# Performance work log

Hardware: AMD Instinct MI355X
Metric: run time of the kernel (lower is better)

## Reference

```python
import jax, jax.numpy as jnp
import numpy as np

N = 50000      # nodes
E = 1600000    # edges (avg degree 32)
F_IN = 512     # in_channels
H = 128        # hidden_channels


def setup_inputs() -> dict:
    key = jax.random.key(0)
    k0, k1, k2, k3 = jax.random.split(key, 4)
    x = jax.random.normal(k0, (N, F_IN), dtype=jnp.float32)
    edge_index = jax.random.randint(k1, (2, E), 0, N, dtype=jnp.int32)
    edge_weight = jnp.ones((E,), dtype=jnp.float32)
    # GCNConv weight (glorot) + bias, Linear weight (xavier) + bias.
    # Stored as [in, out] for direct matmul (same math as torch's x @ W.T).
    W_conv = jax.random.normal(k2, (F_IN, H), dtype=jnp.float32) * np.sqrt(2.0 / (F_IN + H)).astype(np.float32)
    b_conv = jnp.zeros((H,), dtype=jnp.float32)
    W_lin = jax.random.normal(k3, (H, F_IN), dtype=jnp.float32) * np.sqrt(2.0 / (H + F_IN)).astype(np.float32)
    b_lin = jnp.zeros((F_IN,), dtype=jnp.float32)
    return {
        "x": x, "edge_index": edge_index, "edge_weight": edge_weight,
        "W_conv": W_conv, "b_conv": b_conv, "W_lin": W_lin, "b_lin": b_lin,
    }


def reference(x, edge_index, edge_weight, W_conv, b_conv, W_lin, b_lin):
    n = x.shape[0]
    src, dst = edge_index[0], edge_index[1]
    # GCN normalization with self-loops (add_self_loops + sym norm)
    loop = jnp.arange(n, dtype=edge_index.dtype)
    src_f = jnp.concatenate([src, loop])            # [E+N]
    dst_f = jnp.concatenate([dst, loop])
    w = jnp.concatenate([edge_weight, jnp.ones((n,), x.dtype)])
    deg = jax.ops.segment_sum(w, dst_f, num_segments=n)  # [N]
    dinv = jnp.where(deg > 0, jax.lax.rsqrt(deg), 0.0)
    norm = dinv[src_f] * w * dinv[dst_f]            # [E+N]
    # GCNConv: transform then normalized neighbor aggregation
    h = x @ W_conv                                  # [N, H]
    agg = jax.ops.segment_sum(h[src_f] * norm[:, None], dst_f, num_segments=n) + b_conv  # [N, H]
    # dropout p=0.0 (eval) is identity; final linear projection back to F_IN
    return agg @ W_lin + b_lin                      # [N, F_IN]
```

## Files before the change

### kernel.cpp

```cpp
#include <hip/hip_runtime.h>

#define NN 50000
#define EE 1600000
#define FIN 512
#define HH 128

#define CAP 80
#define OVF_CAP 64512

#define GROUP 128
#define NB ((NN + GROUP - 1) / GROUP)
#define NBLK 256
#define EPB (EE / NBLK)

typedef short s16x8 __attribute__((ext_vector_type(8)));
typedef float f32x4 __attribute__((ext_vector_type(4)));

static __device__ inline unsigned short f2bf(float f) {
    unsigned u = __float_as_uint(f);
    unsigned r = (u + 0x7fffu + ((u >> 16) & 1u)) >> 16;
    return (unsigned short)r;
}

static __device__ inline float blo(unsigned u) { return __uint_as_float(u << 16); }
static __device__ inline float bhi(unsigned u) { return __uint_as_float(u & 0xffff0000u); }


__global__ __launch_bounds__(256) void hist_kernel(const int* __restrict__ dst,
                                                   int* __restrict__ hist) {
    __shared__ int h[NB];
    const int tid = threadIdx.x;
    for (int i = tid; i < NB; i += 256) h[i] = 0;
    __syncthreads();
    const int base = blockIdx.x * EPB;
    for (int i = tid; i < EPB; i += 256)
        atomicAdd(&h[dst[base + i] >> 7], 1);
    __syncthreads();
    for (int i = tid; i < NB; i += 256) hist[blockIdx.x * NB + i] = h[i];
}

__global__ __launch_bounds__(64) void scan_bins(const int* __restrict__ hist,
                                                int* __restrict__ off,
                                                int* __restrict__ binTotal) {
    const int bin = blockIdx.x;
    const int lane = threadIdx.x;
    int v[4];
    int s = 0;
#pragma unroll
    for (int i = 0; i < 4; ++i) { v[i] = hist[(lane * 4 + i) * NB + bin]; s += v[i]; }
    int incl = s;
#pragma unroll
    for (int d = 1; d < 64; d <<= 1) {
        int t = __shfl_up(incl, d, 64);
        if (lane >= d) incl += t;
    }
    int run = incl - s;
#pragma unroll
    for (int i = 0; i < 4; ++i) { off[(lane * 4 + i) * NB + bin] = run; run += v[i]; }
    if (lane == 63) binTotal[bin] = incl;
}

__global__ __launch_bounds__(512) void bin_base(const int* __restrict__ binTotal,
                                                int* __restrict__ binBase) {
    __shared__ int s[512];
    const int t = threadIdx.x;
    int mine = (t < NB) ? binTotal[t] : 0;
    s[t] = mine;
    __syncthreads();
    for (int d = 1; d < 512; d <<= 1) {
        int v = (t >= d) ? s[t - d] : 0;
        __syncthreads();
        s[t] += v;
        __syncthreads();
    }
    if (t < NB) binBase[t] = s[t] - mine;
}

__global__ __launch_bounds__(256) void place_kernel(const int* __restrict__ src,
                                                    const int* __restrict__ dst,
                                                    const float* __restrict__ w,
                                                    const int* __restrict__ off,
                                                    const int* __restrict__ binBase,
                                                    int2* __restrict__ bins) {
    __shared__ int cur[NB];
    const int tid = threadIdx.x;
    for (int i = tid; i < NB; i += 256)
        cur[i] = binBase[i] + off[blockIdx.x * NB + i];
    __syncthreads();
    const int base = blockIdx.x * EPB;
    for (int i = tid; i < EPB; i += 256) {
        int e = base + i;
        int s = src[e], d = dst[e];
        float we = w[e];
        int pos = atomicAdd(&cur[d >> 7], 1);
        bins[pos] = make_int2(s | ((d & 127) << 16), __float_as_int(we));
    }
}

__global__ __launch_bounds__(512) void bucket_build(const int* __restrict__ binBase,
                                                    const int* __restrict__ binTotal,
                                                    const int2* __restrict__ bins,
                                                    int* __restrict__ cnt,
                                                    int2* __restrict__ bucket,
                                                    float* __restrict__ deg,
                                                    int* __restrict__ ovf_cnt,
                                                    int4* __restrict__ ovf) {
    __shared__ int lcnt[GROUP];
    __shared__ float lw[GROUP];
    const int b = blockIdx.x;
    const int tid = threadIdx.x;
    if (tid < GROUP) { lcnt[tid] = 0; lw[tid] = 0.0f; }
    __syncthreads();
    const int base = b * GROUP;
    const int start = binBase[b];
    const int n = binTotal[b];
    for (int i = tid; i < n; i += 512) {
        int2 en = bins[start + i];
        int sr = en.x & 0xffff;
        int dl = (en.x >> 16) & 127;
        int pos = atomicAdd(&lcnt[dl], 1);
        if (pos < CAP) {
            bucket[(size_t)(base + dl) * CAP + pos] = make_int2(sr, en.y);
            atomicAdd(&lw[dl], __int_as_float(en.y));
        } else {
            int o = atomicAdd(ovf_cnt, 1);
            if (o < OVF_CAP) ovf[o] = make_int4(sr, base + dl, en.y, 0);
        }
    }
    __syncthreads();
    for (int i = tid; i < GROUP; i += 512) {
        int node = base + i;
        if (node < NN) {
            cnt[node] = lcnt[i];
            deg[node] = 1.0f + lw[i];
        }
    }
}

__global__ void ovf_deg(const int* __restrict__ ovf_cnt, const int4* __restrict__ ovf,
                        float* __restrict__ deg) {
    int n = min(*ovf_cnt, OVF_CAP);
    for (int i = blockIdx.x * blockDim.x + threadIdx.x; i < n; i += blockDim.x * gridDim.x)
        atomicAdd(deg + ovf[i].y, __int_as_float(ovf[i].z));
}

__global__ void dinv_kernel(const float* __restrict__ deg, float* __restrict__ dinv, int n) {
    int i = blockIdx.x * 256 + threadIdx.x;
    if (i < n) {
        float d = deg[i];
        dinv[i] = (d > 0.0f) ? rsqrtf(d) : 0.0f;
    }
}


__global__ __launch_bounds__(512) void gemm1_kernel(const float* __restrict__ A,
                                                    const float* __restrict__ B,
                                                    const float* __restrict__ dinv,
                                                    unsigned short* __restrict__ h2,
                                                    int M) {
    __shared__ short As[128][40];
    __shared__ short Bs[128][40];
    const int bm = blockIdx.x * 128;
    const int tid = threadIdx.x;
    const int wave = tid >> 6, lane = tid & 63;
    const int wm = wave >> 1, wn = wave & 1;
    const int mlane = lane & 15, quad = lane >> 4;

    const int ar = tid >> 3, akq = tid & 7;
    const int bn = tid & 127, bkg = tid >> 7;

    f32x4 acc[2][4];
#pragma unroll
    for (int i = 0; i < 2; ++i)
#pragma unroll
        for (int j = 0; j < 4; ++j) acc[i][j] = (f32x4){0.f, 0.f, 0.f, 0.f};

    float4 pa0[2], pa1[2];
    float pb0[8], pb1[8];

    auto loadT = [&](float4 (&pa)[2], float (&pb)[8], int k0) {
#pragma unroll
        for (int i = 0; i < 2; ++i) {
            int grow = bm + ar + i * 64;
            pa[i] = make_float4(0.f, 0.f, 0.f, 0.f);
            if (grow < M) pa[i] = *(const float4*)(A + (size_t)grow * FIN + k0 + akq * 4);
        }
#pragma unroll
        for (int j = 0; j < 8; ++j)
            pb[j] = B[(size_t)(k0 + bkg * 8 + j) * HH + bn];
    };
    auto storeT = [&](float4 (&pa)[2], float (&pb)[8]) {
#pragma unroll
        for (int i = 0; i < 2; ++i) {
            ushort4 b;
            b.x = f2bf(pa[i].x); b.y = f2bf(pa[i].y); b.z = f2bf(pa[i].z); b.w = f2bf(pa[i].w);
            *(ushort4*)&As[ar + i * 64][akq * 4] = b;
        }
        unsigned short tmp[8];
#pragma unroll
        for (int j = 0; j < 8; ++j) tmp[j] = f2bf(pb[j]);
        *(s16x8*)&Bs[bn][bkg * 8] = *(s16x8*)tmp;
    };
    auto mmaT = [&]() {
        s16x8 af[2], bfr[4];
#pragma unroll
        for (int mt = 0; mt < 2; ++mt)
            af[mt] = *(const s16x8*)&As[wm * 32 + mt * 16 + mlane][quad * 8];
#pragma unroll
        for (int nt = 0; nt < 4; ++nt)
            bfr[nt] = *(const s16x8*)&Bs[wn * 64 + nt * 16 + mlane][quad * 8];
#pragma unroll
        for (int mt = 0; mt < 2; ++mt)
#pragma unroll
            for (int nt = 0; nt < 4; ++nt)
                acc[mt][nt] = __builtin_amdgcn_mfma_f32_16x16x32_bf16(af[mt], bfr[nt], acc[mt][nt], 0, 0, 0);
    };

    loadT(pa0, pb0, 0);
    loadT(pa1, pb1, 32);
    for (int kk = 0; kk < 16; kk += 2) {
        storeT(pa0, pb0);
        __syncthreads();
        if (kk + 2 < 16) loadT(pa0, pb0, (kk + 2) * 32);
        mmaT();
        __syncthreads();
        storeT(pa1, pb1);
        __syncthreads();
        if (kk + 3 < 16) loadT(pa1, pb1, (kk + 3) * 32);
        mmaT();
        __syncthreads();
    }

#pragma unroll
    for (int mt = 0; mt < 2; ++mt) {
#pragma unroll
        for (int r = 0; r < 4; ++r) {
            int row = bm + wm * 32 + mt * 16 + quad * 4 + r;
            if (row < M) {
                float sc = dinv[row];
#pragma unroll
                for (int nt = 0; nt < 4; ++nt) {
                    int col = wn * 64 + nt * 16 + mlane;
                    h2[(size_t)row * HH + col] = f2bf(acc[mt][nt][r] * sc);
                }
            }
        }
    }
}


__global__ __launch_bounds__(256) void agg_kernel(const unsigned int* __restrict__ h2u,
                                                  const int* __restrict__ cnt,
                                                  const int2* __restrict__ bucket,
                                                  const float* __restrict__ dinv,
                                                  const float* __restrict__ b_conv,
                                                  const int* __restrict__ ovf_cnt,
                                                  const int4* __restrict__ ovf,
                                                  unsigned int* __restrict__ aggu, int n) {
    int idx = blockIdx.x * 256 + threadIdx.x;
    int node = idx >> 6;
    int lane = idx & 63;
    if (node >= n) return;
    int c = min(cnt[node], CAP);
    const int2* e = bucket + (size_t)node * CAP;

    unsigned self = h2u[(size_t)node * 64 + lane];
    float a0 = blo(self), a1 = bhi(self);
    float b0 = 0.0f, b1 = 0.0f;

    int j = 0;
    for (; j + 8 <= c; j += 8) {
        int4 p0 = *(const int4*)(e + j);
        int4 p1 = *(const int4*)(e + j + 2);
        int4 p2 = *(const int4*)(e + j + 4);
        int4 p3 = *(const int4*)(e + j + 6);
        unsigned u0 = h2u[(size_t)p0.x * 64 + lane];
        unsigned u1 = h2u[(size_t)p0.z * 64 + lane];
        unsigned u2 = h2u[(size_t)p1.x * 64 + lane];
        unsigned u3 = h2u[(size_t)p1.z * 64 + lane];
        unsigned u4 = h2u[(size_t)p2.x * 64 + lane];
        unsigned u5 = h2u[(size_t)p2.z * 64 + lane];
        unsigned u6 = h2u[(size_t)p3.x * 64 + lane];
        unsigned u7 = h2u[(size_t)p3.z * 64 + lane];
        float w0 = __int_as_float(p0.y), w1 = __int_as_float(p0.w);
        float w2 = __int_as_float(p1.y), w3 = __int_as_float(p1.w);
        float w4 = __int_as_float(p2.y), w5 = __int_as_float(p2.w);
        float w6 = __int_as_float(p3.y), w7 = __int_as_float(p3.w);
        a0 += w0 * blo(u0); a1 += w0 * bhi(u0);
        b0 += w1 * blo(u1); b1 += w1 * bhi(u1);
        a0 += w2 * blo(u2); a1 += w2 * bhi(u2);
        b0 += w3 * blo(u3); b1 += w3 * bhi(u3);
        a0 += w4 * blo(u4); a1 += w4 * bhi(u4);
        b0 += w5 * blo(u5); b1 += w5 * bhi(u5);
        a0 += w6 * blo(u6); a1 += w6 * bhi(u6);
        b0 += w7 * blo(u7); b1 += w7 * bhi(u7);
    }
    for (; j + 2 <= c; j += 2) {
        int4 p = *(const int4*)(e + j);
        unsigned u0 = h2u[(size_t)p.x * 64 + lane];
        unsigned u1 = h2u[(size_t)p.z * 64 + lane];
        float w0 = __int_as_float(p.y), w1 = __int_as_float(p.w);
        a0 += w0 * blo(u0); a1 += w0 * bhi(u0);
        b0 += w1 * blo(u1); b1 += w1 * bhi(u1);
    }
    if (j < c) {
        int2 p = e[j];
        float w0 = __int_as_float(p.y);
        unsigned u0 = h2u[(size_t)p.x * 64 + lane];
        a0 += w0 * blo(u0); a1 += w0 * bhi(u0);
    }

    int ovf_n = min(*ovf_cnt, OVF_CAP);
    for (int i = 0; i < ovf_n; ++i) {
        int4 v = ovf[i];
        if (v.y == node) {
            float w0 = __int_as_float(v.z);
            unsigned u0 = h2u[(size_t)v.x * 64 + lane];
            a0 += w0 * blo(u0); a1 += w0 * bhi(u0);
        }
    }

    float di = dinv[node];
    float2 bc = *(const float2*)&b_conv[lane * 2];
    float v0 = bc.x + di * (a0 + b0);
    float v1 = bc.y + di * (a1 + b1);
    aggu[(size_t)node * 64 + lane] = (unsigned)f2bf(v0) | ((unsigned)f2bf(v1) << 16);
}


__global__ __launch_bounds__(256) void gemm2_kernel(const unsigned short* __restrict__ A,
                                                    const float* __restrict__ B,
                                                    const float* __restrict__ bias,
                                                    float* __restrict__ C,
                                                    int M) {
    __shared__ short As[128][40];
    __shared__ short Bs[128][40];
    const int bm = blockIdx.x * 128;
    const int bn = blockIdx.y * 128;
    const int tid = threadIdx.x;
    const int wave = tid >> 6, lane = tid & 63;
    const int wm = wave >> 1, wn = wave & 1;
    const int mlane = lane & 15, quad = lane >> 4;

    f32x4 acc[4][4];
#pragma unroll
    for (int i = 0; i < 4; ++i)
#pragma unroll
        for (int j = 0; j < 4; ++j) acc[i][j] = (f32x4){0.f, 0.f, 0.f, 0.f};

    for (int k0 = 0; k0 < HH; k0 += 32) {
#pragma unroll
        for (int i = 0; i < 2; ++i) {
            int task = tid + i * 256;
            int row = task >> 2, ch = task & 3;
            int grow = bm + row;
            s16x8 v = (s16x8){0, 0, 0, 0, 0, 0, 0, 0};
            if (grow < M) v = *(const s16x8*)(A + (size_t)grow * HH + k0 + ch * 8);
            *(s16x8*)&As[row][ch * 8] = v;
        }
#pragma unroll
        for (int i = 0; i < 2; ++i) {
            int task = tid + i * 256;
            int n = task & 127, kg = task >> 7;
            unsigned short tmp[8];
#pragma unroll
            for (int j = 0; j < 8; ++j)
                tmp[j] = f2bf(B[(size_t)(k0 + kg * 8 + j) * FIN + bn + n]);
            *(s16x8*)&Bs[n][kg * 8] = *(s16x8*)tmp;
        }
        __syncthreads();

        s16x8 af[4], bfr[4];
#pragma unroll
        for (int mt = 0; mt < 4; ++mt)
            af[mt] = *(const s16x8*)&As[wm * 64 + mt * 16 + mlane][quad * 8];
#pragma unroll
        for (int nt = 0; nt < 4; ++nt)
            bfr[nt] = *(const s16x8*)&Bs[wn * 64 + nt * 16 + mlane][quad * 8];
#pragma unroll
        for (int mt = 0; mt < 4; ++mt)
#pragma unroll
            for (int nt = 0; nt < 4; ++nt)
                acc[mt][nt] = __builtin_amdgcn_mfma_f32_16x16x32_bf16(af[mt], bfr[nt], acc[mt][nt], 0, 0, 0);
        __syncthreads();
    }

#pragma unroll
    for (int mt = 0; mt < 4; ++mt) {
#pragma unroll
        for (int r = 0; r < 4; ++r) {
            int row = bm + wm * 64 + mt * 16 + quad * 4 + r;
            if (row < M) {
#pragma unroll
                for (int nt = 0; nt < 4; ++nt) {
                    int col = bn + wn * 64 + nt * 16 + mlane;
                    C[(size_t)row * FIN + col] = acc[mt][nt][r] + bias[col];
                }
            }
        }
    }
}


extern "C" void kernel_launch(void* const* d_in, const int* in_sizes, int n_in,
                              void* d_out, int out_size, void* d_ws, size_t ws_size,
                              hipStream_t stream) {
    const float* x      = (const float*)d_in[0];
    const int*   ei     = (const int*)d_in[1];
    const float* ew     = (const float*)d_in[2];
    const float* W_conv = (const float*)d_in[3];
    const float* b_conv = (const float*)d_in[4];
    const float* W_lin  = (const float*)d_in[5];
    const float* b_lin  = (const float*)d_in[6];
    float* out = (float*)d_out;

    const int* src = ei;
    const int* dst = ei + EE;

    char* ws = (char*)d_ws;
    int*            cnt      = (int*)           (ws + 0);
    float*          deg      = (float*)         (ws + 200704);
    float*          dinv     = (float*)         (ws + 401408);
    int*            ovf_cnt  = (int*)           (ws + 602112);
    int*            binTotal = (int*)           (ws + 602368);
    int*            binBase  = (int*)           (ws + 604160);
    int4*           ovf      = (int4*)          (ws + 605952);
    int2*           bucket   = (int2*)          (ws + 1650944);
    unsigned short* h2       = (unsigned short*)(ws + 33650944);
    unsigned short* agg      = (unsigned short*)(ws + 46450944);

    int*            hist     = (int*)           (ws + 1650944);
    int*            off      = (int*)           (ws + 2051584);
    int2*           bins     = (int2*)          (ws + 33650944);

    hipMemsetAsync(ovf_cnt, 0, sizeof(int), stream);

    const int nb_n = (NN + 255) / 256;
    const int nb_w = (NN * 64 + 255) / 256;

    hist_kernel<<<NBLK, 256, 0, stream>>>(dst, hist);
    scan_bins<<<NB, 64, 0, stream>>>(hist, off, binTotal);
    bin_base<<<1, 512, 0, stream>>>(binTotal, binBase);
    place_kernel<<<NBLK, 256, 0, stream>>>(src, dst, ew, off, binBase, bins);
    bucket_build<<<NB, 512, 0, stream>>>(binBase, binTotal, bins, cnt, bucket, deg, ovf_cnt, ovf);
    ovf_deg<<<4, 256, 0, stream>>>(ovf_cnt, ovf, deg);
    dinv_kernel<<<nb_n, 256, 0, stream>>>(deg, dinv, NN);

    gemm1_kernel<<<dim3((NN + 127) / 128, 1), 512, 0, stream>>>(x, W_conv, dinv, h2, NN);

    agg_kernel<<<nb_w, 256, 0, stream>>>((const unsigned int*)h2, cnt, bucket, dinv, b_conv,
                                         ovf_cnt, ovf, (unsigned int*)agg, NN);

    gemm2_kernel<<<dim3((NN + 127) / 128, FIN / 128), 256, 0, stream>>>(agg, W_lin, b_lin, out, NN);
}
```

Before: 354.0 us.

## Fold dinv into consumers and register-prefetch pipeline gemm2 with 512 threads

Removes the separate dinv kernel; gemm1 and agg_kernel now compute rsqrt of the degree inline, saving one launch and a small global round trip. gemm2 is restructured to 512 threads (8 waves, each handling 32x64 outputs) with a two-stage register prefetch of A and B tiles, so the global loads for the next k-step overlap the MFMA work. This mirrors the gemm1 pipeline and lowers per-thread accumulators, in exchange for more barriers and extra rsqrt work per read.

```diff
diff --git a/kernel.cpp b/kernel.cpp
--- a/kernel.cpp
+++ b/kernel.cpp
@@ -24,6 +24,8 @@
 
 static __device__ inline float blo(unsigned u) { return __uint_as_float(u << 16); }
 static __device__ inline float bhi(unsigned u) { return __uint_as_float(u & 0xffff0000u); }
+
+static __device__ inline float deg2dinv(float d) { return (d > 0.0f) ? rsqrtf(d) : 0.0f; }
 
 
 __global__ __launch_bounds__(256) void hist_kernel(const int* __restrict__ dst,
@@ -144,18 +146,10 @@
         atomicAdd(deg + ovf[i].y, __int_as_float(ovf[i].z));
 }
 
-__global__ void dinv_kernel(const float* __restrict__ deg, float* __restrict__ dinv, int n) {
-    int i = blockIdx.x * 256 + threadIdx.x;
-    if (i < n) {
-        float d = deg[i];
-        dinv[i] = (d > 0.0f) ? rsqrtf(d) : 0.0f;
-    }
-}
-
 
 __global__ __launch_bounds__(512) void gemm1_kernel(const float* __restrict__ A,
                                                     const float* __restrict__ B,
-                                                    const float* __restrict__ dinv,
+                                                    const float* __restrict__ deg,
                                                     unsigned short* __restrict__ h2,
                                                     int M) {
     __shared__ short As[128][40];
@@ -237,7 +231,7 @@
         for (int r = 0; r < 4; ++r) {
             int row = bm + wm * 32 + mt * 16 + quad * 4 + r;
             if (row < M) {
-                float sc = dinv[row];
+                float sc = deg2dinv(deg[row]);
 #pragma unroll
                 for (int nt = 0; nt < 4; ++nt) {
                     int col = wn * 64 + nt * 16 + mlane;
@@ -252,7 +246,7 @@
 __global__ __launch_bounds__(256) void agg_kernel(const unsigned int* __restrict__ h2u,
                                                   const int* __restrict__ cnt,
                                                   const int2* __restrict__ bucket,
-                                                  const float* __restrict__ dinv,
+                                                  const float* __restrict__ deg,
                                                   const float* __restrict__ b_conv,
                                                   const int* __restrict__ ovf_cnt,
                                                   const int4* __restrict__ ovf,
@@ -320,7 +314,7 @@
         }
     }
 
-    float di = dinv[node];
+    float di = deg2dinv(deg[node]);
     float2 bc = *(const float2*)&b_conv[lane * 2];
     float v0 = bc.x + di * (a0 + b0);
     float v1 = bc.y + di * (a1 + b1);
@@ -328,7 +322,7 @@
 }
 
 
-__global__ __launch_bounds__(256) void gemm2_kernel(const unsigned short* __restrict__ A,
+__global__ __launch_bounds__(512) void gemm2_kernel(const unsigned short* __restrict__ A,
                                                     const float* __restrict__ B,
                                                     const float* __restrict__ bias,
                                                     float* __restrict__ C,
@@ -336,64 +330,78 @@
     __shared__ short As[128][40];
     __shared__ short Bs[128][40];
     const int bm = blockIdx.x * 128;
-    const int bn = blockIdx.y * 128;
+    const int bnb = blockIdx.y * 128;
     const int tid = threadIdx.x;
     const int wave = tid >> 6, lane = tid & 63;
     const int wm = wave >> 1, wn = wave & 1;
     const int mlane = lane & 15, quad = lane >> 4;
 
-    f32x4 acc[4][4];
-#pragma unroll
-    for (int i = 0; i < 4; ++i)
+    const int ar = tid >> 2, ach = tid & 3;
+    const int bn = tid & 127, bkg = tid >> 7;
+
+    f32x4 acc[2][4];
+#pragma unroll
+    for (int i = 0; i < 2; ++i)
 #pragma unroll
         for (int j = 0; j < 4; ++j) acc[i][j] = (f32x4){0.f, 0.f, 0.f, 0.f};
 
-    for (int k0 = 0; k0 < HH; k0 += 32) {
-#pragma unroll
-        for (int i = 0; i < 2; ++i) {
-            int task = tid + i * 256;
-            int row = task >> 2, ch = task & 3;
-            int grow = bm + row;
-            s16x8 v = (s16x8){0, 0, 0, 0, 0, 0, 0, 0};
-            if (grow < M) v = *(const s16x8*)(A + (size_t)grow * HH + k0 + ch * 8);
-            *(s16x8*)&As[row][ch * 8] = v;
-        }
-#pragma unroll
-        for (int i = 0; i < 2; ++i) {
-            int task = tid + i * 256;
-            int n = task & 127, kg = task >> 7;
-            unsigned short tmp[8];
-#pragma unroll
-            for (int j = 0; j < 8; ++j)
-                tmp[j] = f2bf(B[(size_t)(k0 + kg * 8 + j) * FIN + bn + n]);
-            *(s16x8*)&Bs[n][kg * 8] = *(s16x8*)tmp;
-        }
-        __syncthreads();
-
-        s16x8 af[4], bfr[4];
-#pragma unroll
-        for (int mt = 0; mt < 4; ++mt)
-            af[mt] = *(const s16x8*)&As[wm * 64 + mt * 16 + mlane][quad * 8];
+    s16x8 pa0, pa1;
+    float pb0[8], pb1[8];
+
+    auto loadT = [&](s16x8& pa, float (&pb)[8], int k0) {
+        int grow = bm + ar;
+        pa = (s16x8){0, 0, 0, 0, 0, 0, 0, 0};
+        if (grow < M) pa = *(const s16x8*)(A + (size_t)grow * HH + k0 + ach * 8);
+#pragma unroll
+        for (int j = 0; j < 8; ++j)
+            pb[j] = B[(size_t)(k0 + bkg * 8 + j) * FIN + bnb + bn];
+    };
+    auto storeT = [&](s16x8& pa, float (&pb)[8]) {
+        *(s16x8*)&As[ar][ach * 8] = pa;
+        unsigned short tmp[8];
+#pragma unroll
+        for (int j = 0; j < 8; ++j) tmp[j] = f2bf(pb[j]);
+        *(s16x8*)&Bs[bn][bkg * 8] = *(s16x8*)tmp;
+    };
+    auto mmaT = [&]() {
+        s16x8 af[2], bfr[4];
+#pragma unroll
+        for (int mt = 0; mt < 2; ++mt)
+            af[mt] = *(const s16x8*)&As[wm * 32 + mt * 16 + mlane][quad * 8];
 #pragma unroll
         for (int nt = 0; nt < 4; ++nt)
             bfr[nt] = *(const s16x8*)&Bs[wn * 64 + nt * 16 + mlane][quad * 8];
 #pragma unroll
-        for (int mt = 0; mt < 4; ++mt)
+        for (int mt = 0; mt < 2; ++mt)
 #pragma unroll
             for (int nt = 0; nt < 4; ++nt)
                 acc[mt][nt] = __builtin_amdgcn_mfma_f32_16x16x32_bf16(af[mt], bfr[nt], acc[mt][nt], 0, 0, 0);
-        __syncthreads();
-    }
-
-#pragma unroll
-    for (int mt = 0; mt < 4; ++mt) {
+    };
+
+    loadT(pa0, pb0, 0);
+    loadT(pa1, pb1, 32);
+    for (int kk = 0; kk < 4; kk += 2) {
+        storeT(pa0, pb0);
+        __syncthreads();
+        if (kk + 2 < 4) loadT(pa0, pb0, (kk + 2) * 32);
+        mmaT();
+        __syncthreads();
+        storeT(pa1, pb1);
+        __syncthreads();
+        if (kk + 3 < 4) loadT(pa1, pb1, (kk + 3) * 32);
+        mmaT();
+        __syncthreads();
+    }
+
+#pragma unroll
+    for (int mt = 0; mt < 2; ++mt) {
 #pragma unroll
         for (int r = 0; r < 4; ++r) {
-            int row = bm + wm * 64 + mt * 16 + quad * 4 + r;
+            int row = bm + wm * 32 + mt * 16 + quad * 4 + r;
             if (row < M) {
 #pragma unroll
                 for (int nt = 0; nt < 4; ++nt) {
-                    int col = bn + wn * 64 + nt * 16 + mlane;
+                    int col = bnb + wn * 64 + nt * 16 + mlane;
                     C[(size_t)row * FIN + col] = acc[mt][nt][r] + bias[col];
                 }
             }
@@ -420,7 +428,6 @@
     char* ws = (char*)d_ws;
     int*            cnt      = (int*)           (ws + 0);
     float*          deg      = (float*)         (ws + 200704);
-    float*          dinv     = (float*)         (ws + 401408);
     int*            ovf_cnt  = (int*)           (ws + 602112);
     int*            binTotal = (int*)           (ws + 602368);
     int*            binBase  = (int*)           (ws + 604160);
@@ -435,7 +442,6 @@
 
     hipMemsetAsync(ovf_cnt, 0, sizeof(int), stream);
 
-    const int nb_n = (NN + 255) / 256;
     const int nb_w = (NN * 64 + 255) / 256;
 
     hist_kernel<<<NBLK, 256, 0, stream>>>(dst, hist);
@@ -444,12 +450,11 @@
     place_kernel<<<NBLK, 256, 0, stream>>>(src, dst, ew, off, binBase, bins);
     bucket_build<<<NB, 512, 0, stream>>>(binBase, binTotal, bins, cnt, bucket, deg, ovf_cnt, ovf);
     ovf_deg<<<4, 256, 0, stream>>>(ovf_cnt, ovf, deg);
-    dinv_kernel<<<nb_n, 256, 0, stream>>>(deg, dinv, NN);
-
-    gemm1_kernel<<<dim3((NN + 127) / 128, 1), 512, 0, stream>>>(x, W_conv, dinv, h2, NN);
-
-    agg_kernel<<<nb_w, 256, 0, stream>>>((const unsigned int*)h2, cnt, bucket, dinv, b_conv,
+
+    gemm1_kernel<<<dim3((NN + 127) / 128, 1), 512, 0, stream>>>(x, W_conv, deg, h2, NN);
+
+    agg_kernel<<<nb_w, 256, 0, stream>>>((const unsigned int*)h2, cnt, bucket, deg, b_conv,
                                          ovf_cnt, ovf, (unsigned int*)agg, NN);
 
-    gemm2_kernel<<<dim3((NN + 127) / 128, FIN / 128), 256, 0, stream>>>(agg, W_lin, b_lin, out, NN);
-}
+    gemm2_kernel<<<dim3((NN + 127) / 128, FIN / 128), 512, 0, stream>>>(agg, W_lin, b_lin, out, NN);
+}
```

After: 349.1 us. About the same (-1.4%).
